# Kernel tuning notes

Measured on AMD Instinct MI355X. Metric: run time of the kernel, lower is better.

Reference implementation:

```python
import jax, jax.numpy as jnp
import numpy as np

NUM_BEAMS = 4
EOS = 2
PAD = 0
T = 16  # max_tokens decode steps
NEG = jnp.float32(-1e32)


def setup_inputs() -> dict:
    key = jax.random.key(0)
    ks = jax.random.split(key, 12)
    Vv, E, D, L, bs = 32000, 512, 512, 2, 16
    s = 0.05
    n = lambda k, sh: (jax.random.normal(k, sh, dtype=jnp.float32) * s)
    return {
        'inputs': jax.random.randint(ks[0], (1, bs), 0, Vv),
        'h0': n(ks[1], (L, bs, D)),
        'c0': n(ks[2], (L, bs, D)),
        'emb': n(ks[3], (Vv, E)),
        'Wih0': n(ks[4], (4 * D, E)),
        'Whh0': n(ks[5], (4 * D, D)),
        'b0': n(ks[6], (4 * D,)),
        'Wih1': n(ks[7], (4 * D, D)),
        'Whh1': n(ks[8], (4 * D, D)),
        'b1': n(ks[9], (4 * D,)),
        'Wp': n(ks[10], (D, Vv)),
        'bp': n(ks[11], (Vv,)),
    }


def _lstm(x, h, c, Wih, Whh, b):
    z = x @ Wih.T + h @ Whh.T + b
    i, f, g, o = jnp.split(z, 4, axis=-1)
    c = jax.nn.sigmoid(f) * c + jax.nn.sigmoid(i) * jnp.tanh(g)
    h = jax.nn.sigmoid(o) * jnp.tanh(c)
    return h, c


def reference(inputs, h0, c0, emb, Wih0, Whh0, b0, Wih1, Whh1, b1, Wp, bp):
    bs = inputs.shape[1]
    nb = NUM_BEAMS
    B = bs * nb
    Vv = emb.shape[0]

    def cell(tok, h, c):
        # one decode step of the 2-layer LSTM + projection; tok: (B,)
        x = emb[tok]
        h0n, c0n = _lstm(x, h[0], c[0], Wih0, Whh0, b0)
        h1n, c1n = _lstm(h0n, h[1], c[1], Wih1, Whh1, b1)
        logits = h1n @ Wp + bp  # (B, V)
        return logits, jnp.stack([h0n, h1n]), jnp.stack([c0n, c1n])

    offs = jnp.arange(bs)[:, None] * nb  # batch-major beam layout b*nb+beam

    # ---- iteration 0: all beams identical, keep beam 0 only ----
    tokens = jnp.repeat(inputs[0], nb)           # (B,)
    h = jnp.repeat(h0, nb, axis=1)               # (L, B, D)
    c = jnp.repeat(c0, nb, axis=1)
    logits0, h, c = cell(tokens, h, c)
    lp0 = jax.nn.log_softmax(logits0, axis=-1).reshape(bs, nb, Vv)[:, 0, :]
    logprobs, beams = jax.lax.top_k(lp0, nb)     # (bs, nb)
    pidx = (beams // Vv + offs).reshape(-1)      # parents == 0
    tokens = (beams % Vv).reshape(-1)
    h = h[:, pidx]
    c = c[:, pidx]
    finished = tokens == EOS
    beam_out = jnp.zeros((T + 1, B), dtype=tokens.dtype)
    beam_out = beam_out.at[0].set(jnp.repeat(inputs[0], nb)[pidx]).at[1].set(tokens)

    # ---- iterations 1..T-1 ----
    def step(carry, t):
        tokens, h, c, logprobs, finished, beam_out = carry
        logits, h, c = cell(tokens, h, c)
        new_lp = jax.nn.log_softmax(logits, axis=-1).reshape(bs, nb, Vv) + logprobs[:, :, None]
        # finished beams: forced to emit PAD with unchanged cumulative logprob
        masked = jnp.full((bs, nb, Vv), NEG).at[:, :, PAD].set(logprobs)
        fin = finished.reshape(bs, nb)
        new_lp = jnp.where(fin[:, :, None], masked, new_lp)
        logprobs, beams = jax.lax.top_k(new_lp.reshape(bs, nb * Vv), nb)
        pidx = (beams // Vv + offs).reshape(-1)
        toks = (beams % Vv).reshape(-1)
        h = h[:, pidx]
        c = c[:, pidx]
        finished = finished[pidx] | (toks == EOS)
        beam_out = beam_out[:, pidx].at[t + 1].set(toks)
        return (toks, h, c, logprobs, finished, beam_out), logits

    carry0 = (tokens, h, c, logprobs, finished, beam_out)
    carry_f, logits_seq = jax.lax.scan(step, carry0, jnp.arange(1, T))
    logits_all = jnp.concatenate([logits0[None], logits_seq], axis=0)  # (T, B, V)
    beam_outputs = carry_f[5].reshape(T + 1, bs, nb)
    return logits_all, beam_outputs
```

## Files before the change

### kernel.cpp

```cpp
#include <hip/hip_runtime.h>
#include <math.h>

#define BS     16
#define NB     4
#define BB     64
#define DD     512
#define VV     32000
#define TSTEPS 16
#define EOSTOK 2
#define NEGF   (-1e32f)
#define VT     64
#define NVT    (VV / VT)

__device__ __forceinline__ bool better(float av, int ai, float bv, int bi_) {
    return (av > bv) || (av == bv && ai < bi_);
}

__device__ __forceinline__ void glds4(const float* src, float* dst) {
    __builtin_amdgcn_global_load_lds((const __attribute__((address_space(1))) void*)src,
                                     (__attribute__((address_space(3))) void*)dst, 4, 0, 0);
}
__device__ __forceinline__ void glds16(const float* src, float* dst) {
    __builtin_amdgcn_global_load_lds((const __attribute__((address_space(1))) void*)src,
                                     (__attribute__((address_space(3))) void*)dst, 16, 0, 0);
}

__global__ void init_kernel(const int* __restrict__ inputs,
                            const float* __restrict__ h0, const float* __restrict__ c0,
                            float* __restrict__ h0s, float* __restrict__ c0s,
                            float* __restrict__ h1s, float* __restrict__ c1s,
                            int* __restrict__ tokens, int* __restrict__ pidx,
                            int* __restrict__ fin, float* __restrict__ lp,
                            int* __restrict__ bo)
{
    int tid = blockIdx.x * blockDim.x + threadIdx.x;
    int total = BB * DD;
    for (int i = tid; i < total; i += gridDim.x * blockDim.x) {
        int b = i / DD;
        int d = i % DD;
        int src0 = 0 * BS * DD + (b >> 2) * DD + d;
        int src1 = 1 * BS * DD + (b >> 2) * DD + d;
        h0s[i] = h0[src0];
        c0s[i] = c0[src0];
        h1s[i] = h0[src1];
        c1s[i] = c0[src1];
    }
    if (tid < BB) {
        tokens[tid] = inputs[tid >> 2];
        pidx[tid]   = tid;
        fin[tid]    = 0;
        lp[tid]     = 0.0f;
        bo[0 * BB + tid] = inputs[tid >> 2];
        for (int r = 1; r <= TSTEPS; r++) bo[r * BB + tid] = 0;
    }
}

__global__ __launch_bounds__(256) void lstm_kernel(
    const float* __restrict__ xbase, const int* __restrict__ xrow,
    const float* __restrict__ hsrc,  const float* __restrict__ csrc,
    const int* __restrict__ prow,
    float* __restrict__ hdst, float* __restrict__ cdst,
    const float* __restrict__ Wih, const float* __restrict__ Whh,
    const float* __restrict__ bias)
{
    __shared__ float U[64][129];
    __shared__ float Wl[4][1024];
    __shared__ double Z[4][64];
    __shared__ int rows_s[64], prows_s[64];
    int tid = threadIdx.x;
    int j = blockIdx.x;
    int b = tid & 63;
    int g = tid >> 6;
    int lane = tid & 63;
    int w = tid >> 6;

    #pragma unroll
    for (int i = 0; i < 4; i++) {
        int s0 = i * 256 + w * 64;
        int gg = s0 >> 8;
        int hh = (s0 >> 7) & 1;
        int c0 = s0 & 127;
        const float* rowbase = (hh ? Whh : Wih) + (size_t)(gg * DD + j) * DD;
        glds16(rowbase + 4 * (c0 + lane), (float*)Wl + 4 * s0);
    }
    if (tid < 64) {
        rows_s[tid]  = xrow ? xrow[tid] : tid;
        prows_s[tid] = prow[tid];
    }

    double a0 = 0.0, a1 = 0.0, a2 = 0.0, a3 = 0.0;
    for (int ch = 0; ch < 8; ch++) {
        int k0 = ch * 128;
        __syncthreads();
        #pragma unroll
        for (int i = 0; i < 32; i++) {
            int e0 = i * 256 + w * 64;
            int bb = e0 >> 7;
            int kk0 = e0 & 127;
            const float* src;
            if (k0 < 512) src = xbase + (size_t)rows_s[bb] * DD + k0 + kk0 + lane;
            else          src = hsrc + (size_t)prows_s[bb] * DD + (k0 - 512) + kk0 + lane;
            glds4(src, &U[bb][kk0]);
        }
        __syncthreads();
        const float* Wrow = &Wl[g][k0];
        #pragma unroll 8
        for (int kk = 0; kk < 128; kk += 4) {
            a0 = fma((double)U[b][kk + 0], (double)Wrow[kk + 0], a0);
            a1 = fma((double)U[b][kk + 1], (double)Wrow[kk + 1], a1);
            a2 = fma((double)U[b][kk + 2], (double)Wrow[kk + 2], a2);
            a3 = fma((double)U[b][kk + 3], (double)Wrow[kk + 3], a3);
        }
    }
    Z[g][b] = ((a0 + a1) + (a2 + a3));
    __syncthreads();

    if (tid < 64) {
        double zi = Z[0][b] + (double)bias[0 * DD + j];
        double zf = Z[1][b] + (double)bias[1 * DD + j];
        double zg = Z[2][b] + (double)bias[2 * DD + j];
        double zo = Z[3][b] + (double)bias[3 * DD + j];
        double si = 1.0 / (1.0 + exp(-zi));
        double sf = 1.0 / (1.0 + exp(-zf));
        double so = 1.0 / (1.0 + exp(-zo));
        double cold = (double)csrc[(size_t)prows_s[b] * DD + j];
        double cn = sf * cold + si * tanh(zg);
        double hn = so * tanh(cn);
        hdst[b * DD + j] = (float)hn;
        cdst[b * DD + j] = (float)cn;
    }
}

__global__ __launch_bounds__(256) void proj_kernel(
    const float* __restrict__ h1, const float* __restrict__ Wp,
    double* __restrict__ pp)
{
    __shared__ float sh[64][68];
    __shared__ float sw[64][68];
    int vtile = blockIdx.x % NVT;
    int kh    = blockIdx.x / NVT;
    int kbase = kh * 256;
    int vbase = vtile * VT;
    int tid = threadIdx.x;
    int lane = tid & 63;
    int w = tid >> 6;
    int b0 = (tid >> 4) * 4;
    int v0 = (tid & 15) * 4;

    double acc[4][4];
    #pragma unroll
    for (int i = 0; i < 4; i++)
        #pragma unroll
        for (int q = 0; q < 4; q++) acc[i][q] = 0.0;

    for (int ch = 0; ch < 4; ch++) {
        int k0 = kbase + ch * 64;
        __syncthreads();
        #pragma unroll
        for (int i = 0; i < 16; i++) {
            int bb = i * 4 + w;
            glds4(h1 + (size_t)bb * DD + k0 + lane, &sh[bb][0]);
        }
        #pragma unroll
        for (int i = 0; i < 16; i++) {
            int kk = i * 4 + w;
            glds4(Wp + (size_t)(k0 + kk) * VV + vbase + lane, &sw[kk][0]);
        }
        __syncthreads();
        #pragma unroll
        for (int k4 = 0; k4 < 16; k4++) {
            int k = k4 * 4;
            float4 h4[4], w4[4];
            #pragma unroll
            for (int i = 0; i < 4; i++) h4[i] = *(const float4*)&sh[b0 + i][k];
            #pragma unroll
            for (int kk = 0; kk < 4; kk++) w4[kk] = *(const float4*)&sw[k + kk][v0];
            #pragma unroll
            for (int i = 0; i < 4; i++) {
                const float hh[4] = {h4[i].x, h4[i].y, h4[i].z, h4[i].w};
                #pragma unroll
                for (int kk = 0; kk < 4; kk++) {
                    double hd = (double)hh[kk];
                    const float ww[4] = {w4[kk].x, w4[kk].y, w4[kk].z, w4[kk].w};
                    #pragma unroll
                    for (int q = 0; q < 4; q++)
                        acc[i][q] = fma(hd, (double)ww[q], acc[i][q]);
                }
            }
        }
    }

    double* base = pp + (size_t)kh * BB * VV;
    #pragma unroll
    for (int i = 0; i < 4; i++)
        #pragma unroll
        for (int q = 0; q < 4; q++)
            base[(size_t)(b0 + i) * VV + vbase + v0 + q] = acc[i][q];
}

#define NPT 32
__global__ __launch_bounds__(1024) void row_kernel(
    const double* __restrict__ pp, const float* __restrict__ bp,
    float* __restrict__ outf, const float* __restrict__ lp,
    const int* __restrict__ fin,
    float* __restrict__ rcv, int* __restrict__ rci, int step0)
{
    int row = blockIdx.x;
    int j   = row & 3;
    int tid = threadIdx.x;
    int base_idx = j * VV;

    const double* p0 = pp + (size_t)row * VV;
    const double* p1 = pp + (size_t)BB * VV + (size_t)row * VV;
    float* xo = outf + (size_t)row * VV;

    __shared__ double red[1024];

    float zreg[NPT];
    double m = -1e300;
    #pragma unroll
    for (int q = 0; q < NPT; q++) {
        int i = tid + q * 1024;
        float zf = 0.0f;
        if (i < VV) {
            double z = (p0[i] + p1[i]) + (double)bp[i];
            zf = (float)z;
            xo[i] = zf;
            m = fmax(m, (double)zf);
        }
        zreg[q] = zf;
    }

    float lp_r = step0 ? 0.0f : lp[row];
    int   f    = step0 ? 0    : fin[row];
    if (step0 && j != 0) {
        if (tid < 4) { rcv[row * 4 + tid] = NEGF; rci[row * 4 + tid] = base_idx + tid; }
        return;
    }
    if (f) {
        if (tid < 4) {
            rcv[row * 4 + tid] = (tid == 0) ? lp_r : NEGF;
            rci[row * 4 + tid] = base_idx + tid;
        }
        return;
    }

    red[tid] = m; __syncthreads();
    for (int s = 512; s > 0; s >>= 1) {
        if (tid < s) red[tid] = fmax(red[tid], red[tid + s]);
        __syncthreads();
    }
    m = red[0];
    __syncthreads();

    double sum = 0.0;
    #pragma unroll
    for (int q = 0; q < NPT; q++) {
        int i = tid + q * 1024;
        if (i < VV) sum += exp((double)zreg[q] - m);
    }
    red[tid] = sum; __syncthreads();
    for (int s = 512; s > 0; s >>= 1) {
        if (tid < s) red[tid] += red[tid + s];
        __syncthreads();
    }
    double lse = m + log(red[0]);
    __syncthreads();

    float bv[4]; int bx[4];
    #pragma unroll
    for (int q = 0; q < 4; q++) { bv[q] = -3.4e38f; bx[q] = 0x7fffffff; }
    #pragma unroll
    for (int q = 0; q < NPT; q++) {
        int i = tid + q * 1024;
        if (i < VV) {
            float lgp32 = (float)((double)zreg[q] - lse);
            float val   = (float)((double)lp_r + (double)lgp32);
            int idx = base_idx + i;
            if (better(val, idx, bv[3], bx[3])) {
                bv[3] = val; bx[3] = idx;
                #pragma unroll
                for (int s = 3; s > 0; s--) {
                    if (better(bv[s], bx[s], bv[s - 1], bx[s - 1])) {
                        float tv2 = bv[s]; bv[s] = bv[s - 1]; bv[s - 1] = tv2;
                        int ti2 = bx[s]; bx[s] = bx[s - 1]; bx[s - 1] = ti2;
                    }
                }
            }
        }
    }

    __shared__ float sv[1024][4];
    __shared__ int   si_[1024][4];
    #pragma unroll
    for (int q = 0; q < 4; q++) { sv[tid][q] = bv[q]; si_[tid][q] = bx[q]; }
    __syncthreads();
    for (int s = 512; s > 0; s >>= 1) {
        if (tid < s) {
            float av[4], ov[4], mv[4]; int ai[4], oi[4], mi[4];
            #pragma unroll
            for (int q = 0; q < 4; q++) {
                av[q] = sv[tid][q];     ai[q] = si_[tid][q];
                ov[q] = sv[tid + s][q]; oi[q] = si_[tid + s][q];
            }
            int pa = 0, pb = 0;
            #pragma unroll
            for (int q = 0; q < 4; q++) {
                bool takeA = (pb >= 4) || (pa < 4 && better(av[pa], ai[pa], ov[pb], oi[pb]));
                if (takeA) { mv[q] = av[pa]; mi[q] = ai[pa]; pa++; }
                else       { mv[q] = ov[pb]; mi[q] = oi[pb]; pb++; }
            }
            #pragma unroll
            for (int q = 0; q < 4; q++) { sv[tid][q] = mv[q]; si_[tid][q] = mi[q]; }
        }
        __syncthreads();
    }
    if (tid < 4) {
        rcv[row * 4 + tid] = sv[0][tid];
        rci[row * 4 + tid] = si_[0][tid];
    }
}

__global__ void merge_update_kernel(
    const float* __restrict__ rcv, const int* __restrict__ rci,
    float* __restrict__ lp, int* __restrict__ fin,
    int* __restrict__ tokens, int* __restrict__ pidx,
    int* __restrict__ bo, int t)
{
    int b = threadIdx.x;
    int bi = b >> 2, r = b & 3;

    float cv[16]; int ci[16];
    #pragma unroll
    for (int c = 0; c < 16; c++) { cv[c] = rcv[bi * 16 + c]; ci[c] = rci[bi * 16 + c]; }

    int sel = 0;
    #pragma unroll
    for (int c = 0; c < 16; c++) {
        int rank = 0;
        #pragma unroll
        for (int d = 0; d < 16; d++)
            if (d != c && better(cv[d], ci[d], cv[c], ci[c])) rank++;
        if (rank == r) sel = c;
    }

    float v = cv[sel];
    int flat = ci[sel];
    int q = flat / VV;
    int p = q + bi * 4;
    int tok = flat - q * VV;
    int oldfin = fin[p];
    int col[TSTEPS + 1];
    #pragma unroll
    for (int rr = 0; rr <= TSTEPS; rr++) col[rr] = bo[rr * BB + p];
    __syncthreads();
    #pragma unroll
    for (int rr = 0; rr <= TSTEPS; rr++) bo[rr * BB + b] = col[rr];
    bo[(t + 1) * BB + b] = tok;
    fin[b]    = oldfin | (tok == EOSTOK);
    lp[b]     = v;
    tokens[b] = tok;
    pidx[b]   = p;
}

__global__ void final_kernel(const int* __restrict__ bo, float* __restrict__ out)
{
    int i = blockIdx.x * blockDim.x + threadIdx.x;
    if (i < (TSTEPS + 1) * BB) out[i] = (float)bo[i];
}

extern "C" void kernel_launch(void* const* d_in, const int* in_sizes, int n_in,
                              void* d_out, int out_size, void* d_ws, size_t ws_size,
                              hipStream_t stream)
{
    const int*   inputs = (const int*)d_in[0];
    const float* h0   = (const float*)d_in[1];
    const float* c0   = (const float*)d_in[2];
    const float* emb  = (const float*)d_in[3];
    const float* Wih0 = (const float*)d_in[4];
    const float* Whh0 = (const float*)d_in[5];
    const float* b0   = (const float*)d_in[6];
    const float* Wih1 = (const float*)d_in[7];
    const float* Whh1 = (const float*)d_in[8];
    const float* b1   = (const float*)d_in[9];
    const float* Wp   = (const float*)d_in[10];
    const float* bp   = (const float*)d_in[11];
    float* out = (float*)d_out;

    char* w = (char*)d_ws;
    size_t off = 0;
    auto alloc = [&](size_t bytes) { void* p = w + off; off += (bytes + 255) & ~255ULL; return p; };
    double* pp = (double*)alloc((size_t)2 * BB * VV * 8);
    float* h0s[2], *c0s[2], *h1s[2], *c1s[2];
    for (int s = 0; s < 2; s++) {
        h0s[s] = (float*)alloc(BB * DD * 4);
        c0s[s] = (float*)alloc(BB * DD * 4);
        h1s[s] = (float*)alloc(BB * DD * 4);
        c1s[s] = (float*)alloc(BB * DD * 4);
    }
    float* rcv   = (float*)alloc(BB * 4 * 4);
    int*   rci   = (int*)alloc(BB * 4 * 4);
    float* lp    = (float*)alloc(BB * 4);
    int* pidx    = (int*)alloc(BB * 4);
    int* tokens  = (int*)alloc(BB * 4);
    int* fin     = (int*)alloc(BB * 4);
    int* bo      = (int*)alloc((TSTEPS + 1) * BB * 4);

    init_kernel<<<128, 256, 0, stream>>>(inputs, h0, c0,
                                         h0s[0], c0s[0], h1s[0], c1s[0],
                                         tokens, pidx, fin, lp, bo);

    for (int t = 0; t < TSTEPS; t++) {
        int s = t & 1, d2 = s ^ 1;
        lstm_kernel<<<512, 256, 0, stream>>>(emb, tokens, h0s[s], c0s[s], pidx,
                                             h0s[d2], c0s[d2], Wih0, Whh0, b0);
        lstm_kernel<<<512, 256, 0, stream>>>(h0s[d2], nullptr, h1s[s], c1s[s], pidx,
                                             h1s[d2], c1s[d2], Wih1, Whh1, b1);

        float* outf = out + (size_t)t * BB * VV;
        proj_kernel<<<NVT * 2, 256, 0, stream>>>(h1s[d2], Wp, pp);
        row_kernel<<<BB, 1024, 0, stream>>>(pp, bp, outf, lp, fin, rcv, rci, t == 0 ? 1 : 0);
        merge_update_kernel<<<1, 64, 0, stream>>>(rcv, rci, lp, fin, tokens, pidx, bo, t);
    }
    final_kernel<<<5, 256, 0, stream>>>(bo, out + (size_t)TSTEPS * BB * VV);
}
```

Before: 3.061 ms.

## Drop split-K in projection, write biased float logits directly

The projection kernel now runs the full K=512 reduction in each block instead of splitting K across two blocks that write double partials to a workspace. Bias is added in the projection epilogue and float logits go straight to the output. The row kernel reads those logits back and skips finished or inactive rows before loading. This removes the large double-precision partial buffer traffic, but halves the grid (500 blocks) and doubles per-block work. Summation order changes slightly, since K is no longer combined as two halves, which could shift ties in top-k.

```diff
diff --git a/kernel.cpp b/kernel.cpp
--- a/kernel.cpp
+++ b/kernel.cpp
@@ -133,14 +133,11 @@
 
 __global__ __launch_bounds__(256) void proj_kernel(
     const float* __restrict__ h1, const float* __restrict__ Wp,
-    double* __restrict__ pp)
+    const float* __restrict__ bp, float* __restrict__ outf)
 {
     __shared__ float sh[64][68];
     __shared__ float sw[64][68];
-    int vtile = blockIdx.x % NVT;
-    int kh    = blockIdx.x / NVT;
-    int kbase = kh * 256;
-    int vbase = vtile * VT;
+    int vbase = blockIdx.x * VT;
     int tid = threadIdx.x;
     int lane = tid & 63;
     int w = tid >> 6;
@@ -153,8 +150,8 @@
         #pragma unroll
         for (int q = 0; q < 4; q++) acc[i][q] = 0.0;
 
-    for (int ch = 0; ch < 4; ch++) {
-        int k0 = kbase + ch * 64;
+    for (int ch = 0; ch < 8; ch++) {
+        int k0 = ch * 64;
         __syncthreads();
         #pragma unroll
         for (int i = 0; i < 16; i++) {
@@ -190,18 +187,20 @@
         }
     }
 
-    double* base = pp + (size_t)kh * BB * VV;
-    #pragma unroll
-    for (int i = 0; i < 4; i++)
-        #pragma unroll
-        for (int q = 0; q < 4; q++)
-            base[(size_t)(b0 + i) * VV + vbase + v0 + q] = acc[i][q];
+    #pragma unroll
+    for (int i = 0; i < 4; i++) {
+        int brow = b0 + i;
+        #pragma unroll
+        for (int q = 0; q < 4; q++) {
+            int v = vbase + v0 + q;
+            outf[(size_t)brow * VV + v] = (float)(acc[i][q] + (double)bp[v]);
+        }
+    }
 }
 
 #define NPT 32
 __global__ __launch_bounds__(1024) void row_kernel(
-    const double* __restrict__ pp, const float* __restrict__ bp,
-    float* __restrict__ outf, const float* __restrict__ lp,
+    const float* __restrict__ outf, const float* __restrict__ lp,
     const int* __restrict__ fin,
     float* __restrict__ rcv, int* __restrict__ rci, int step0)
 {
@@ -209,27 +208,6 @@
     int j   = row & 3;
     int tid = threadIdx.x;
     int base_idx = j * VV;
-
-    const double* p0 = pp + (size_t)row * VV;
-    const double* p1 = pp + (size_t)BB * VV + (size_t)row * VV;
-    float* xo = outf + (size_t)row * VV;
-
-    __shared__ double red[1024];
-
-    float zreg[NPT];
-    double m = -1e300;
-    #pragma unroll
-    for (int q = 0; q < NPT; q++) {
-        int i = tid + q * 1024;
-        float zf = 0.0f;
-        if (i < VV) {
-            double z = (p0[i] + p1[i]) + (double)bp[i];
-            zf = (float)z;
-            xo[i] = zf;
-            m = fmax(m, (double)zf);
-        }
-        zreg[q] = zf;
-    }
 
     float lp_r = step0 ? 0.0f : lp[row];
     int   f    = step0 ? 0    : fin[row];
@@ -243,6 +221,22 @@
             rci[row * 4 + tid] = base_idx + tid;
         }
         return;
+    }
+
+    const float* xo = outf + (size_t)row * VV;
+    __shared__ double red[1024];
+
+    float zreg[NPT];
+    double m = -1e300;
+    #pragma unroll
+    for (int q = 0; q < NPT; q++) {
+        int i = tid + q * 1024;
+        float zf = 0.0f;
+        if (i < VV) {
+            zf = xo[i];
+            m = fmax(m, (double)zf);
+        }
+        zreg[q] = zf;
     }
 
     red[tid] = m; __syncthreads();
@@ -390,7 +384,6 @@
     char* w = (char*)d_ws;
     size_t off = 0;
     auto alloc = [&](size_t bytes) { void* p = w + off; off += (bytes + 255) & ~255ULL; return p; };
-    double* pp = (double*)alloc((size_t)2 * BB * VV * 8);
     float* h0s[2], *c0s[2], *h1s[2], *c1s[2];
     for (int s = 0; s < 2; s++) {
         h0s[s] = (float*)alloc(BB * DD * 4);
@@ -418,8 +411,8 @@
                                              h1s[d2], c1s[d2], Wih1, Whh1, b1);
 
         float* outf = out + (size_t)t * BB * VV;
-        proj_kernel<<<NVT * 2, 256, 0, stream>>>(h1s[d2], Wp, pp);
-        row_kernel<<<BB, 1024, 0, stream>>>(pp, bp, outf, lp, fin, rcv, rci, t == 0 ? 1 : 0);
+        proj_kernel<<<NVT, 256, 0, stream>>>(h1s[d2], Wp, bp, outf);
+        row_kernel<<<BB, 1024, 0, stream>>>(outf, lp, fin, rcv, rci, t == 0 ? 1 : 0);
         merge_update_kernel<<<1, 64, 0, stream>>>(rcv, rci, lp, fin, tokens, pidx, bo, t);
     }
     final_kernel<<<5, 256, 0, stream>>>(bo, out + (size_t)TSTEPS * BB * VV);
```

Result: faster. 2.851 ms (-6.9%).
